# Kernel tuning notes

Measured on AMD Instinct MI355X. Metric: run time of the kernel, lower is better.

Reference implementation:

```python
import jax, jax.numpy as jnp
import numpy as np

B, C, T, N = 8, 128, 64, 256
D_STATE, D_CONV, EXPAND = 4, 3, 1
D_INNER = EXPAND * C
DT_RANK = (C + 15) // 16  # 8


def setup_inputs() -> dict:
    key = jax.random.key(0)
    ks = jax.random.split(key, 8)
    s = lambda k, shape, sc=0.02: jax.random.normal(k, shape, jnp.float32) * sc
    return {
        "x": jax.random.normal(ks[0], (B, C, T, N), jnp.float32),
        "ln_gamma": jnp.ones((C,), jnp.float32),
        "ln_beta": jnp.zeros((C,), jnp.float32),
        "in_proj_w": s(ks[1], (2 * D_INNER, C)),
        "conv_w": s(ks[2], (D_CONV, 1, D_INNER), 0.1),
        "conv_b": jnp.zeros((D_INNER,), jnp.float32),
        "x_proj_w": s(ks[3], (DT_RANK + 2 * D_STATE, D_INNER)),
        "dt_proj_w": s(ks[4], (D_INNER, DT_RANK), 0.1),
        "dt_proj_b": s(ks[5], (D_INNER,), 0.1),
        "A_log": jnp.log(jnp.broadcast_to(jnp.arange(1, D_STATE + 1, dtype=jnp.float32), (D_INNER, D_STATE))),
        "D": jnp.ones((D_INNER,), jnp.float32),
        "out_proj_w": s(ks[6], (C, D_INNER)),
    }


def _mamba(x, in_proj_w, conv_w, conv_b, x_proj_w, dt_proj_w, dt_proj_b, A_log, D, out_proj_w):
    # x: (BN, T, C) -- selective-scan Mamba block, single (forward) direction
    xz = x @ in_proj_w.T                                   # (BN, T, 2*D_INNER)
    xc, z = jnp.split(xz, 2, axis=-1)
    # causal depthwise conv along time
    xp = jnp.pad(xc, ((0, 0), (D_CONV - 1, 0), (0, 0)))
    xc = jax.lax.conv_general_dilated(
        xp, conv_w, (1,), 'VALID',
        dimension_numbers=('NWC', 'WIO', 'NWC'),
        feature_group_count=D_INNER) + conv_b
    xc = jax.nn.silu(xc)
    x_dbl = xc @ x_proj_w.T                                # (BN, T, DT_RANK + 2*D_STATE)
    dt, Bs, Cs = jnp.split(x_dbl, [DT_RANK, DT_RANK + D_STATE], axis=-1)
    dt = jax.nn.softplus(dt @ dt_proj_w.T + dt_proj_b)     # (BN, T, D_INNER)
    A = -jnp.exp(A_log)                                    # (D_INNER, D_STATE)
    dA = jnp.exp(dt[..., None] * A)                        # (BN, T, D_INNER, D_STATE)
    dBx = dt[..., None] * Bs[:, :, None, :] * xc[..., None]

    def step(h, inps):
        dA_t, dBx_t, C_t = inps
        h = h * dA_t + dBx_t                               # (BN, D_INNER, D_STATE)
        y = jnp.einsum('bdn,bn->bd', h, C_t)
        return h, y

    h0 = jnp.zeros((xc.shape[0], D_INNER, D_STATE), xc.dtype)
    _, ys = jax.lax.scan(step, h0, (dA.transpose(1, 0, 2, 3),
                                    dBx.transpose(1, 0, 2, 3),
                                    Cs.transpose(1, 0, 2)))
    y = ys.transpose(1, 0, 2) + xc * D                     # (BN, T, D_INNER)
    y = y * jax.nn.silu(z)                                 # gate (if_divide_out=False)
    return y @ out_proj_w.T


def reference(x, ln_gamma, ln_beta, in_proj_w, conv_w, conv_b, x_proj_w,
              dt_proj_w, dt_proj_b, A_log, D, out_proj_w):
    # (B, C, T, N) -> (B, T, N, C)
    h = x.transpose(0, 2, 3, 1)
    mu = h.mean(-1, keepdims=True)
    var = h.var(-1, keepdims=True)
    h = (h - mu) / jnp.sqrt(var + 1e-5) * ln_gamma + ln_beta
    h = h.astype(jnp.float32)  # fp32 cast (autocast disabled around mamba)
    bb, tt, nn, cc = h.shape
    # temporal mode: each (batch, node) pair is an independent time sequence
    hs = h.transpose(0, 2, 1, 3).reshape(bb * nn, tt, cc)
    y = _mamba(hs, in_proj_w, conv_w, conv_b, x_proj_w, dt_proj_w, dt_proj_b,
               A_log, D, out_proj_w)
    y = y.reshape(bb, nn, tt, cc).transpose(0, 2, 1, 3)    # (B, T, N, C)
    return y.transpose(0, 3, 1, 2)                         # (B, C, T, N)
```

## Files before the change

kernel.cpp:

```cpp
#include <hip/hip_runtime.h>
#include <math.h>

#define B_   8
#define C_   128
#define T_   64
#define N_   256
#define NSEQ 4

typedef __attribute__((ext_vector_type(8))) short bf16x8;
typedef __attribute__((ext_vector_type(4))) float f32x4;
typedef unsigned short ushort_t;

#define LOG2E 1.4426950408889634f
#define LN2   0.6931471805599453f

#define R0   0
#define R1   8448
#define RXD  17024
#define LDSW 18304

#define SELH 0x05040100u
#define SELL 0x07060302u

__device__ __forceinline__ unsigned bfhi(float x) {
  unsigned u = __float_as_uint(x);
  return (u + 0x7FFF + ((u >> 16) & 1)) >> 16;
}
__device__ __forceinline__ unsigned packsplit(float x) {
  unsigned hi = bfhi(x);
  float rem = x - __uint_as_float(hi << 16);
  unsigned lo = bfhi(rem);
  return (hi & 0xFFFFu) | (lo << 16);
}
__device__ __forceinline__ float unpacksplit(unsigned u) {
  return __uint_as_float(u << 16) + __uint_as_float(u & 0xFFFF0000u);
}
__device__ __forceinline__ float fsilu(float v) {
  return v * __builtin_amdgcn_rcpf(1.0f + __builtin_amdgcn_exp2f(-LOG2E * v));
}
__device__ __forceinline__ float qsum4(float v) {
  int x = __builtin_amdgcn_update_dpp(0, __float_as_int(v), 0xB1, 0xF, 0xF, true);
  v += __int_as_float(x);
  x = __builtin_amdgcn_update_dpp(0, __float_as_int(v), 0x4E, 0xF, 0xF, true);
  v += __int_as_float(x);
  return v;
}
__device__ __forceinline__ int sigq(int qk) { return (qk >> 1) | ((qk & 1) << 2); }
__device__ __forceinline__ int kpos(int k, int s) {
  return (k & ~31) + ((((sigq((k >> 2) & 7)) + s) & 7) << 2) + (k & 3);
}
union BU { uint4 q; bf16x8 v; unsigned u[4]; };

__global__ __launch_bounds__(512) void k_wsplit(const float* __restrict__ Win,
                                                const float* __restrict__ Wout,
                                                const float* __restrict__ Wx,
                                                ushort_t* __restrict__ wsi,
                                                ushort_t* __restrict__ wso,
                                                ushort_t* __restrict__ wsx) {
  int idx = blockIdx.x * 512 + threadIdx.x;
  const float* src;
  ushort_t* dst;
  if (idx < 1024) {
    int row = idx >> 2, kc = idx & 3;
    src = Win + row * 128 + kc * 32;
    dst = wsi + (row * 4 + kc) * 64;
  } else if (idx < 1536) {
    int k = idx - 1024;
    int row = k >> 2, kc = k & 3;
    src = Wout + row * 128 + kc * 32;
    dst = wso + (row * 4 + kc) * 64;
  } else if (idx < 1600) {
    int k = idx - 1536;
    int row = k >> 2, kc = k & 3;
    src = Wx + row * 128 + kc * 32;
    dst = wsx + (row * 4 + kc) * 64;
  } else {
    return;
  }
  for (int g = 0; g < 4; ++g) {
    unsigned hw[4], lw[4];
#pragma unroll
    for (int e2 = 0; e2 < 4; ++e2) {
      float x0 = src[g * 8 + 2 * e2], x1 = src[g * 8 + 2 * e2 + 1];
      unsigned p0 = packsplit(x0), p1 = packsplit(x1);
      hw[e2] = (p0 & 0xFFFFu) | (p1 << 16);
      lw[e2] = (p0 >> 16) | (p1 & 0xFFFF0000u);
    }
    *(uint4*)(dst + (g * 2 + 0) * 8) = make_uint4(hw[0], hw[1], hw[2], hw[3]);
    *(uint4*)(dst + (g * 2 + 1) * 8) = make_uint4(lw[0], lw[1], lw[2], lw[3]);
  }
}

__global__ __launch_bounds__(256) void k_ln(const float* __restrict__ x,
                                            const float* __restrict__ gam,
                                            const float* __restrict__ bet,
                                            float* __restrict__ hout) {
  __shared__ float tile[128 * 36];
  __shared__ float ps[8 * 32], pq[8 * 32], mean_s[32], rstd_s[32];
  int bx = blockIdx.x;
  int nt = bx & 7, t = (bx >> 3) & 63, b = bx >> 9;
  int n0 = nt * 32;
  int tid = threadIdx.x;
  const float4* x4 = (const float4*)x;
  for (int it = 0; it < 4; ++it) {
    int idx4 = it * 256 + tid;
    int c = idx4 >> 3, nn4 = idx4 & 7;
    float4 v = x4[((b * C_ + c) * T_ + t) * (N_ / 4) + (n0 >> 2) + nn4];
    *(float4*)&tile[c * 36 + nn4 * 4] = v;
  }
  __syncthreads();
  {
    int nn = tid & 31, cg = tid >> 5;
    float s = 0.f, q = 0.f;
    for (int i = 0; i < 16; ++i) {
      float v = tile[(cg * 16 + i) * 36 + nn];
      s += v; q += v * v;
    }
    ps[cg * 32 + nn] = s; pq[cg * 32 + nn] = q;
  }
  __syncthreads();
  if (tid < 32) {
    float ss = 0.f, qq = 0.f;
    for (int g2 = 0; g2 < 8; ++g2) { ss += ps[g2 * 32 + tid]; qq += pq[g2 * 32 + tid]; }
    float mu = ss * (1.f / 128.f);
    float var = qq * (1.f / 128.f) - mu * mu;
    mean_s[tid] = mu;
    rstd_s[tid] = rsqrtf(var + 1e-5f);
  }
  __syncthreads();
  {
    int c = tid & 127, half = tid >> 7;
    float gm = gam[c], bb = bet[c];
    for (int it = 0; it < 16; ++it) {
      int n = it * 2 + half;
      float v = (tile[c * 36 + n] - mean_s[n]) * rstd_s[n] * gm + bb;
      hout[((b * N_ + n0 + n) * (long)T_ + t) * C_ + c] = v;
    }
  }
}

__global__ __launch_bounds__(512, 4) void k_mamba(
    float* ws,
    const ushort_t* __restrict__ wsi,
    const ushort_t* __restrict__ wso,
    const ushort_t* __restrict__ wsx,
    const float* __restrict__ convw,
    const float* __restrict__ convb,
    const float* __restrict__ Wdt,
    const float* __restrict__ bdt,
    const float* __restrict__ Alog,
    const float* __restrict__ Dp)
{
  extern __shared__ float L[];
  unsigned* Li = (unsigned*)L;
  int tid = threadIdx.x;
  int lane = tid & 63;
  int w = tid >> 6;
  int r16 = lane & 15, g = lane >> 4;
  const uint4* wsi4 = (const uint4*)wsi;
  const uint4* wso4 = (const uint4*)wso;
  const uint4* wsx4 = (const uint4*)wsx;

  uint4 wih[2][4], wil[2][4], woh[4], wol[4];
#pragma unroll
  for (int ci = 0; ci < 2; ++ci)
#pragma unroll
    for (int kc = 0; kc < 4; ++kc) {
      int cb = ((w * 32 + ci * 16 + r16) * 4 + kc) * 8 + g * 2;
      wih[ci][kc] = wsi4[cb];
      wil[ci][kc] = wsi4[cb + 1];
    }
#pragma unroll
  for (int kc = 0; kc < 4; ++kc) {
    int cb = ((w * 16 + r16) * 4 + kc) * 8 + g * 2;
    woh[kc] = wso4[cb];
    wol[kc] = wso4[cb + 1];
  }
  int dc = tid & 127;
  float cw0 = convw[dc], cw1 = convw[128 + dc], cw2 = convw[256 + dc];
  float cbv = convb[dc];
  int ds = tid >> 2, ss = tid & 3;
  float wA = Wdt[ds * 8 + 2 * ss], wB = Wdt[ds * 8 + 2 * ss + 1];
  float bd = bdt[ds];
  float As2 = -expf(Alog[ds * 4 + ss]) * LOG2E;
  float Dd = Dp[ds];
  int kc_d = (ds & ~31) + (ds & 3);
  int qs_d = sigq((ds >> 2) & 7);

  for (int iseq = 0; iseq < NSEQ; ++iseq) {
    float* hseq = ws + ((long)blockIdx.x * NSEQ + iseq) * (T_ * C_);

    {
      const float4* h4 = (const float4*)hseq;
      int ts = tid >> 3, kg = tid & 7;
      int s = ts & 7;
      int slot = (sigq(kg) + s) & 7;
#pragma unroll
      for (int q = 0; q < 4; ++q) {
        float4 v = h4[ts * 32 + kg + 8 * q];
        uint4 pw = make_uint4(packsplit(v.x), packsplit(v.y), packsplit(v.z), packsplit(v.w));
        *(uint4*)&Li[R0 + ts * 132 + q * 32 + slot * 4] = pw;
      }
    }
    __syncthreads();

    f32x4 acc[4][2];
#pragma unroll
    for (int rt = 0; rt < 4; ++rt)
#pragma unroll
      for (int ci = 0; ci < 2; ++ci) acc[rt][ci] = (f32x4){0.f, 0.f, 0.f, 0.f};
    {
      int s = r16 & 7;
      int slotA = (g + s) & 7, slotB = (g + 4 + s) & 7;
#pragma unroll
      for (int kc = 0; kc < 4; ++kc) {
#pragma unroll
        for (int rt = 0; rt < 4; ++rt) {
          int base = R0 + (rt * 16 + r16) * 132 + kc * 32;
          uint4 wa = *(const uint4*)&Li[base + slotA * 4];
          uint4 wb = *(const uint4*)&Li[base + slotB * 4];
          BU ah, al;
          ah.u[0] = __builtin_amdgcn_perm(wa.y, wa.x, SELH);
          ah.u[1] = __builtin_amdgcn_perm(wa.w, wa.z, SELH);
          ah.u[2] = __builtin_amdgcn_perm(wb.y, wb.x, SELH);
          ah.u[3] = __builtin_amdgcn_perm(wb.w, wb.z, SELH);
          al.u[0] = __builtin_amdgcn_perm(wa.y, wa.x, SELL);
          al.u[1] = __builtin_amdgcn_perm(wa.w, wa.z, SELL);
          al.u[2] = __builtin_amdgcn_perm(wb.y, wb.x, SELL);
          al.u[3] = __builtin_amdgcn_perm(wb.w, wb.z, SELL);
#pragma unroll
          for (int ci = 0; ci < 2; ++ci) {
            BU bh, bl;
            bh.q = wih[ci][kc];
            bl.q = wil[ci][kc];
            acc[rt][ci] = __builtin_amdgcn_mfma_f32_16x16x32_bf16(al.v, bh.v, acc[rt][ci], 0, 0, 0);
            acc[rt][ci] = __builtin_amdgcn_mfma_f32_16x16x32_bf16(ah.v, bl.v, acc[rt][ci], 0, 0, 0);
            acc[rt][ci] = __builtin_amdgcn_mfma_f32_16x16x32_bf16(ah.v, bh.v, acc[rt][ci], 0, 0, 0);
          }
        }
      }
    }
    __syncthreads();

    {
      int dl0 = (w & 3) * 32;
      if (w < 4) {
#pragma unroll
        for (int rt = 0; rt < 4; ++rt)
#pragma unroll
          for (int ci = 0; ci < 2; ++ci)
#pragma unroll
            for (int r = 0; r < 4; ++r)
              L[R0 + (rt * 16 + g * 4 + r) * 132 + dl0 + ci * 16 + r16] = acc[rt][ci][r];
      } else {
#pragma unroll
        for (int rt = 0; rt < 4; ++rt)
#pragma unroll
          for (int ci = 0; ci < 2; ++ci)
#pragma unroll
            for (int r = 0; r < 4; ++r)
              L[R1 + (dl0 + ci * 16 + r16) * 67 + rt * 16 + g * 4 + r] = fsilu(acc[rt][ci][r]);
      }
    }
    __syncthreads();

    {
      int tq = tid >> 7;
      int t0 = tq * 16;
      float xin[18];
#pragma unroll
      for (int ii = 0; ii < 18; ++ii) {
        int t = t0 - 2 + ii;
        xin[ii] = (t < 0) ? 0.f : L[R0 + t * 132 + dc];
      }
      __syncthreads();
#pragma unroll
      for (int ii = 0; ii < 16; ++ii) {
        int t = t0 + ii;
        float v = fmaf(cw2, xin[ii + 2], fmaf(cw1, xin[ii + 1], fmaf(cw0, xin[ii], cbv)));
        Li[R0 + t * 132 + kpos(dc, t & 7)] = packsplit(fsilu(v));
      }
    }
    __syncthreads();

    if (w < 4) {
      int s = r16 & 7;
      int slotA = (g + s) & 7, slotB = (g + 4 + s) & 7;
      f32x4 o = (f32x4){0.f, 0.f, 0.f, 0.f};
#pragma unroll
      for (int kc = 0; kc < 4; ++kc) {
        int cb = (r16 * 4 + kc) * 8 + g * 2;
        BU bh, bl;
        bh.q = wsx4[cb];
        bl.q = wsx4[cb + 1];
        int base = R0 + (w * 16 + r16) * 132 + kc * 32;
        uint4 wa = *(const uint4*)&Li[base + slotA * 4];
        uint4 wb = *(const uint4*)&Li[base + slotB * 4];
        BU ah, al;
        ah.u[0] = __builtin_amdgcn_perm(wa.y, wa.x, SELH);
        ah.u[1] = __builtin_amdgcn_perm(wa.w, wa.z, SELH);
        ah.u[2] = __builtin_amdgcn_perm(wb.y, wb.x, SELH);
        ah.u[3] = __builtin_amdgcn_perm(wb.w, wb.z, SELH);
        al.u[0] = __builtin_amdgcn_perm(wa.y, wa.x, SELL);
        al.u[1] = __builtin_amdgcn_perm(wa.w, wa.z, SELL);
        al.u[2] = __builtin_amdgcn_perm(wb.y, wb.x, SELL);
        al.u[3] = __builtin_amdgcn_perm(wb.w, wb.z, SELL);
        o = __builtin_amdgcn_mfma_f32_16x16x32_bf16(al.v, bh.v, o, 0, 0, 0);
        o = __builtin_amdgcn_mfma_f32_16x16x32_bf16(ah.v, bl.v, o, 0, 0, 0);
        o = __builtin_amdgcn_mfma_f32_16x16x32_bf16(ah.v, bh.v, o, 0, 0, 0);
      }
      int p = (r16 < 8) ? ((r16 >> 1) * 4 + (r16 & 1))
                        : (r16 < 12 ? (r16 - 8) * 4 + 2 : (r16 - 12) * 4 + 3);
#pragma unroll
      for (int q = 0; q < 4; ++q)
        L[RXD + (w * 16 + g * 4 + q) * 20 + p] = o[q];
    }
    __syncthreads();

    {
      float h = 0.f;
#pragma unroll 8
      for (int t = 0; t < 64; ++t) {
        float4 xd = *(const float4*)&L[RXD + t * 20 + ss * 4];
        float dtv = qsum4(fmaf(xd.x, wA, xd.y * wB)) + bd;
        float e = __builtin_amdgcn_exp2f(dtv * LOG2E);
        float sp = LN2 * __builtin_amdgcn_logf(1.0f + e);
        dtv = (dtv > 20.f) ? dtv : sp;
        int xoff = R0 + t * 132 + kc_d + (((qs_d + (t & 7)) & 7) << 2);
        float xcv = unpacksplit(Li[xoff]);
        float dA = __builtin_amdgcn_exp2f(dtv * As2);
        h = fmaf(h, dA, dtv * xcv * xd.z);
        float y = qsum4(h * xd.w);
        if ((t & 3) == ss) {
          y = fmaf(xcv, Dd, y);
          y *= L[R1 + ds * 67 + t];
          Li[xoff] = packsplit(y);
        }
      }
    }
    __syncthreads();

    {
      int s = r16 & 7;
      int slotA = (g + s) & 7, slotB = (g + 4 + s) & 7;
      f32x4 o[4];
#pragma unroll
      for (int rt = 0; rt < 4; ++rt) o[rt] = (f32x4){0.f, 0.f, 0.f, 0.f};
#pragma unroll
      for (int kc = 0; kc < 4; ++kc) {
        BU bh, bl;
        bh.q = woh[kc];
        bl.q = wol[kc];
#pragma unroll
        for (int rt = 0; rt < 4; ++rt) {
          int base = R0 + (rt * 16 + r16) * 132 + kc * 32;
          uint4 wa = *(const uint4*)&Li[base + slotA * 4];
          uint4 wb = *(const uint4*)&Li[base + slotB * 4];
          BU ah, al;
          ah.u[0] = __builtin_amdgcn_perm(wa.y, wa.x, SELH);
          ah.u[1] = __builtin_amdgcn_perm(wa.w, wa.z, SELH);
          ah.u[2] = __builtin_amdgcn_perm(wb.y, wb.x, SELH);
          ah.u[3] = __builtin_amdgcn_perm(wb.w, wb.z, SELH);
          al.u[0] = __builtin_amdgcn_perm(wa.y, wa.x, SELL);
          al.u[1] = __builtin_amdgcn_perm(wa.w, wa.z, SELL);
          al.u[2] = __builtin_amdgcn_perm(wb.y, wb.x, SELL);
          al.u[3] = __builtin_amdgcn_perm(wb.w, wb.z, SELL);
          o[rt] = __builtin_amdgcn_mfma_f32_16x16x32_bf16(al.v, bh.v, o[rt], 0, 0, 0);
          o[rt] = __builtin_amdgcn_mfma_f32_16x16x32_bf16(ah.v, bl.v, o[rt], 0, 0, 0);
          o[rt] = __builtin_amdgcn_mfma_f32_16x16x32_bf16(ah.v, bh.v, o[rt], 0, 0, 0);
        }
      }
#pragma unroll
      for (int rt = 0; rt < 4; ++rt)
#pragma unroll
        for (int r = 0; r < 4; ++r)
          hseq[(rt * 16 + g * 4 + r) * C_ + w * 16 + r16] = o[rt][r];
    }
    __syncthreads();
  }
}

__global__ __launch_bounds__(256) void k_out_tr(const float* __restrict__ ws_y,
                                                float* __restrict__ out) {
  __shared__ float tile[32 * 132];
  int bx = blockIdx.x;
  int nt = bx & 7, t = (bx >> 3) & 63, b = bx >> 9;
  int n0 = nt * 32;
  int tid = threadIdx.x;
  const float4* y4 = (const float4*)ws_y;
  for (int it = 0; it < 4; ++it) {
    int idx4 = it * 256 + tid;
    int nn = idx4 >> 5, c4 = idx4 & 31;
    float4 v = y4[((b * N_ + n0 + nn) * (long)T_ + t) * (C_ / 4) + c4];
    *(float4*)&tile[nn * 132 + c4 * 4] = v;
  }
  __syncthreads();
  int nn = tid & 31, cg = tid >> 5;
  for (int i = 0; i < 16; ++i) {
    int c = cg * 16 + i;
    out[((b * C_ + c) * (long)T_ + t) * N_ + n0 + nn] = tile[nn * 132 + c];
  }
}

extern "C" void kernel_launch(void* const* d_in, const int* in_sizes, int n_in,
                              void* d_out, int out_size, void* d_ws, size_t ws_size,
                              hipStream_t stream) {
  const float* x    = (const float*)d_in[0];
  const float* gam  = (const float*)d_in[1];
  const float* bet  = (const float*)d_in[2];
  const float* Win  = (const float*)d_in[3];
  const float* cw   = (const float*)d_in[4];
  const float* cb   = (const float*)d_in[5];
  const float* Wx   = (const float*)d_in[6];
  const float* Wdt  = (const float*)d_in[7];
  const float* bdt  = (const float*)d_in[8];
  const float* Alog = (const float*)d_in[9];
  const float* Dp   = (const float*)d_in[10];
  const float* Wout = (const float*)d_in[11];
  float* out = (float*)d_out;
  float* ws  = (float*)d_ws;

  const size_t HBYTES = 67108864ull;
  const size_t WBYTES = 131072ull + 65536ull + 8192ull;
  char* wtail;
  if (ws_size >= HBYTES + WBYTES) wtail = (char*)d_ws + HBYTES;
  else                            wtail = (char*)d_out;
  ushort_t* wsi = (ushort_t*)wtail;
  ushort_t* wso = (ushort_t*)(wtail + 131072);
  ushort_t* wsx = (ushort_t*)(wtail + 131072 + 65536);

  (void)hipFuncSetAttribute((const void*)k_mamba,
                            hipFuncAttributeMaxDynamicSharedMemorySize,
                            LDSW * 4);

  k_wsplit<<<4, 512, 0, stream>>>(Win, Wout, Wx, wsi, wso, wsx);
  k_ln<<<4096, 256, 0, stream>>>(x, gam, bet, ws);
  k_mamba<<<2048 / NSEQ, 512, LDSW * 4, stream>>>(ws, wsi, wso, wsx, cw, cb,
                                                  Wdt, bdt, Alog, Dp);
  k_out_tr<<<4096, 256, 0, stream>>>(ws, out);
}
```

Before: 238.0 us.

## Split hi/lo bf16 planes in LDS, restructure dt computation and scan, reload weights

The input tile is now stored as separate hi and lo bf16 planes in LDS with a padded row stride, so the in-projection MFMA operands load directly without perm-based unpacking. The dt projection is computed once per timestep by one lane of each quad, using all 8 weights, and then broadcast through DPP, replacing the per-step qsum4 reduction. The low halves of the in-proj weights and all out-proj weights are reloaded from global memory inside the loop instead of being held in registers, which lowers register pressure but adds global loads. The x_dbl layout in LDS is simplified to match.

```diff
diff --git a/kernel.cpp b/kernel.cpp
--- a/kernel.cpp
+++ b/kernel.cpp
@@ -14,10 +14,11 @@
 #define LOG2E 1.4426950408889634f
 #define LN2   0.6931471805599453f
 
-#define R0   0
-#define R1   8448
-#define RXD  17024
-#define LDSW 18304
+#define RH   0
+#define RL   4352
+#define R1   8704
+#define RXD  17280
+#define LDSW 18560
 
 #define SELH 0x05040100u
 #define SELL 0x07060302u
@@ -44,6 +45,11 @@
   x = __builtin_amdgcn_update_dpp(0, __float_as_int(v), 0x4E, 0xF, 0xF, true);
   v += __int_as_float(x);
   return v;
+}
+template <int SI>
+__device__ __forceinline__ float qbcast(float v) {
+  constexpr int sel = SI | (SI << 2) | (SI << 4) | (SI << 6);
+  return __int_as_float(__builtin_amdgcn_update_dpp(0, __float_as_int(v), sel, 0xF, 0xF, true));
 }
 __device__ __forceinline__ int sigq(int qk) { return (qk >> 1) | ((qk & 1) << 2); }
 __device__ __forceinline__ int kpos(int k, int s) {
@@ -161,26 +167,19 @@
   const uint4* wso4 = (const uint4*)wso;
   const uint4* wsx4 = (const uint4*)wsx;
 
-  uint4 wih[2][4], wil[2][4], woh[4], wol[4];
+  uint4 wih[2][4];
 #pragma unroll
   for (int ci = 0; ci < 2; ++ci)
 #pragma unroll
-    for (int kc = 0; kc < 4; ++kc) {
-      int cb = ((w * 32 + ci * 16 + r16) * 4 + kc) * 8 + g * 2;
-      wih[ci][kc] = wsi4[cb];
-      wil[ci][kc] = wsi4[cb + 1];
-    }
-#pragma unroll
-  for (int kc = 0; kc < 4; ++kc) {
-    int cb = ((w * 16 + r16) * 4 + kc) * 8 + g * 2;
-    woh[kc] = wso4[cb];
-    wol[kc] = wso4[cb + 1];
-  }
+    for (int kc = 0; kc < 4; ++kc)
+      wih[ci][kc] = wsi4[((w * 32 + ci * 16 + r16) * 4 + kc) * 8 + g * 2];
+
   int dc = tid & 127;
   float cw0 = convw[dc], cw1 = convw[128 + dc], cw2 = convw[256 + dc];
   float cbv = convb[dc];
   int ds = tid >> 2, ss = tid & 3;
-  float wA = Wdt[ds * 8 + 2 * ss], wB = Wdt[ds * 8 + 2 * ss + 1];
+  float4 wdta = *(const float4*)&Wdt[ds * 8];
+  float4 wdtb = *(const float4*)&Wdt[ds * 8 + 4];
   float bd = bdt[ds];
   float As2 = -expf(Alog[ds * 4 + ss]) * LOG2E;
   float Dd = Dp[ds];
@@ -193,14 +192,24 @@
     {
       const float4* h4 = (const float4*)hseq;
       int ts = tid >> 3, kg = tid & 7;
-      int s = ts & 7;
-      int slot = (sigq(kg) + s) & 7;
+      unsigned hw[8], lw[8];
 #pragma unroll
       for (int q = 0; q < 4; ++q) {
-        float4 v = h4[ts * 32 + kg + 8 * q];
-        uint4 pw = make_uint4(packsplit(v.x), packsplit(v.y), packsplit(v.z), packsplit(v.w));
-        *(uint4*)&Li[R0 + ts * 132 + q * 32 + slot * 4] = pw;
-      }
+        float4 v = h4[ts * 32 + kg * 4 + q];
+        unsigned h0 = bfhi(v.x), h1 = bfhi(v.y), h2 = bfhi(v.z), h3 = bfhi(v.w);
+        hw[2 * q]     = h0 | (h1 << 16);
+        hw[2 * q + 1] = h2 | (h3 << 16);
+        float r0 = v.x - __uint_as_float(h0 << 16);
+        float r1 = v.y - __uint_as_float(h1 << 16);
+        float r2 = v.z - __uint_as_float(h2 << 16);
+        float r3 = v.w - __uint_as_float(h3 << 16);
+        lw[2 * q]     = bfhi(r0) | (bfhi(r1) << 16);
+        lw[2 * q + 1] = bfhi(r2) | (bfhi(r3) << 16);
+      }
+      *(uint4*)&Li[RH + ts * 68 + kg * 8]     = make_uint4(hw[0], hw[1], hw[2], hw[3]);
+      *(uint4*)&Li[RH + ts * 68 + kg * 8 + 4] = make_uint4(hw[4], hw[5], hw[6], hw[7]);
+      *(uint4*)&Li[RL + ts * 68 + kg * 8]     = make_uint4(lw[0], lw[1], lw[2], lw[3]);
+      *(uint4*)&Li[RL + ts * 68 + kg * 8 + 4] = make_uint4(lw[4], lw[5], lw[6], lw[7]);
     }
     __syncthreads();
 
@@ -209,35 +218,25 @@
     for (int rt = 0; rt < 4; ++rt)
 #pragma unroll
       for (int ci = 0; ci < 2; ++ci) acc[rt][ci] = (f32x4){0.f, 0.f, 0.f, 0.f};
-    {
-      int s = r16 & 7;
-      int slotA = (g + s) & 7, slotB = (g + 4 + s) & 7;
-#pragma unroll
-      for (int kc = 0; kc < 4; ++kc) {
-#pragma unroll
-        for (int rt = 0; rt < 4; ++rt) {
-          int base = R0 + (rt * 16 + r16) * 132 + kc * 32;
-          uint4 wa = *(const uint4*)&Li[base + slotA * 4];
-          uint4 wb = *(const uint4*)&Li[base + slotB * 4];
-          BU ah, al;
-          ah.u[0] = __builtin_amdgcn_perm(wa.y, wa.x, SELH);
-          ah.u[1] = __builtin_amdgcn_perm(wa.w, wa.z, SELH);
-          ah.u[2] = __builtin_amdgcn_perm(wb.y, wb.x, SELH);
-          ah.u[3] = __builtin_amdgcn_perm(wb.w, wb.z, SELH);
-          al.u[0] = __builtin_amdgcn_perm(wa.y, wa.x, SELL);
-          al.u[1] = __builtin_amdgcn_perm(wa.w, wa.z, SELL);
-          al.u[2] = __builtin_amdgcn_perm(wb.y, wb.x, SELL);
-          al.u[3] = __builtin_amdgcn_perm(wb.w, wb.z, SELL);
-#pragma unroll
-          for (int ci = 0; ci < 2; ++ci) {
-            BU bh, bl;
-            bh.q = wih[ci][kc];
-            bl.q = wil[ci][kc];
-            acc[rt][ci] = __builtin_amdgcn_mfma_f32_16x16x32_bf16(al.v, bh.v, acc[rt][ci], 0, 0, 0);
-            acc[rt][ci] = __builtin_amdgcn_mfma_f32_16x16x32_bf16(ah.v, bl.v, acc[rt][ci], 0, 0, 0);
-            acc[rt][ci] = __builtin_amdgcn_mfma_f32_16x16x32_bf16(ah.v, bh.v, acc[rt][ci], 0, 0, 0);
-          }
-        }
+#pragma unroll
+    for (int kc = 0; kc < 4; ++kc) {
+      BU bl0, bl1, bh0, bh1;
+      bl0.q = wsi4[((w * 32 + r16) * 4 + kc) * 8 + g * 2 + 1];
+      bl1.q = wsi4[((w * 32 + 16 + r16) * 4 + kc) * 8 + g * 2 + 1];
+      bh0.q = wih[0][kc];
+      bh1.q = wih[1][kc];
+#pragma unroll
+      for (int rt = 0; rt < 4; ++rt) {
+        int row = rt * 16 + r16;
+        BU ah, al;
+        ah.q = *(const uint4*)&Li[RH + row * 68 + kc * 16 + g * 4];
+        al.q = *(const uint4*)&Li[RL + row * 68 + kc * 16 + g * 4];
+        acc[rt][0] = __builtin_amdgcn_mfma_f32_16x16x32_bf16(al.v, bh0.v, acc[rt][0], 0, 0, 0);
+        acc[rt][0] = __builtin_amdgcn_mfma_f32_16x16x32_bf16(ah.v, bl0.v, acc[rt][0], 0, 0, 0);
+        acc[rt][0] = __builtin_amdgcn_mfma_f32_16x16x32_bf16(ah.v, bh0.v, acc[rt][0], 0, 0, 0);
+        acc[rt][1] = __builtin_amdgcn_mfma_f32_16x16x32_bf16(al.v, bh1.v, acc[rt][1], 0, 0, 0);
+        acc[rt][1] = __builtin_amdgcn_mfma_f32_16x16x32_bf16(ah.v, bl1.v, acc[rt][1], 0, 0, 0);
+        acc[rt][1] = __builtin_amdgcn_mfma_f32_16x16x32_bf16(ah.v, bh1.v, acc[rt][1], 0, 0, 0);
       }
     }
     __syncthreads();
@@ -251,7 +250,7 @@
           for (int ci = 0; ci < 2; ++ci)
 #pragma unroll
             for (int r = 0; r < 4; ++r)
-              L[R0 + (rt * 16 + g * 4 + r) * 132 + dl0 + ci * 16 + r16] = acc[rt][ci][r];
+              L[(rt * 16 + g * 4 + r) * 132 + dl0 + ci * 16 + r16] = acc[rt][ci][r];
       } else {
 #pragma unroll
         for (int rt = 0; rt < 4; ++rt)
@@ -271,14 +270,14 @@
 #pragma unroll
       for (int ii = 0; ii < 18; ++ii) {
         int t = t0 - 2 + ii;
-        xin[ii] = (t < 0) ? 0.f : L[R0 + t * 132 + dc];
+        xin[ii] = (t < 0) ? 0.f : L[t * 132 + dc];
       }
       __syncthreads();
 #pragma unroll
       for (int ii = 0; ii < 16; ++ii) {
         int t = t0 + ii;
         float v = fmaf(cw2, xin[ii + 2], fmaf(cw1, xin[ii + 1], fmaf(cw0, xin[ii], cbv)));
-        Li[R0 + t * 132 + kpos(dc, t & 7)] = packsplit(fsilu(v));
+        Li[t * 132 + kpos(dc, t & 7)] = packsplit(fsilu(v));
       }
     }
     __syncthreads();
@@ -293,7 +292,7 @@
         BU bh, bl;
         bh.q = wsx4[cb];
         bl.q = wsx4[cb + 1];
-        int base = R0 + (w * 16 + r16) * 132 + kc * 32;
+        int base = (w * 16 + r16) * 132 + kc * 32;
         uint4 wa = *(const uint4*)&Li[base + slotA * 4];
         uint4 wb = *(const uint4*)&Li[base + slotB * 4];
         BU ah, al;
@@ -309,33 +308,51 @@
         o = __builtin_amdgcn_mfma_f32_16x16x32_bf16(ah.v, bl.v, o, 0, 0, 0);
         o = __builtin_amdgcn_mfma_f32_16x16x32_bf16(ah.v, bh.v, o, 0, 0, 0);
       }
-      int p = (r16 < 8) ? ((r16 >> 1) * 4 + (r16 & 1))
-                        : (r16 < 12 ? (r16 - 8) * 4 + 2 : (r16 - 12) * 4 + 3);
 #pragma unroll
       for (int q = 0; q < 4; ++q)
-        L[RXD + (w * 16 + g * 4 + q) * 20 + p] = o[q];
+        L[RXD + (w * 16 + g * 4 + q) * 20 + r16] = o[q];
     }
     __syncthreads();
 
     {
-      float h = 0.f;
-#pragma unroll 8
-      for (int t = 0; t < 64; ++t) {
-        float4 xd = *(const float4*)&L[RXD + t * 20 + ss * 4];
-        float dtv = qsum4(fmaf(xd.x, wA, xd.y * wB)) + bd;
-        float e = __builtin_amdgcn_exp2f(dtv * LOG2E);
+      float hsv = 0.f;
+#pragma unroll
+      for (int tb = 0; tb < 16; ++tb) {
+        int tme = tb * 4 + ss;
+        const float* xr = &L[RXD + tme * 20];
+        float4 xa = *(const float4*)xr;
+        float4 xb = *(const float4*)(xr + 4);
+        float dot = bd;
+        dot = fmaf(xa.x, wdta.x, dot); dot = fmaf(xa.y, wdta.y, dot);
+        dot = fmaf(xa.z, wdta.z, dot); dot = fmaf(xa.w, wdta.w, dot);
+        dot = fmaf(xb.x, wdtb.x, dot); dot = fmaf(xb.y, wdtb.y, dot);
+        dot = fmaf(xb.z, wdtb.z, dot); dot = fmaf(xb.w, wdtb.w, dot);
+        float e = __builtin_amdgcn_exp2f(dot * LOG2E);
         float sp = LN2 * __builtin_amdgcn_logf(1.0f + e);
-        dtv = (dtv > 20.f) ? dtv : sp;
-        int xoff = R0 + t * 132 + kc_d + (((qs_d + (t & 7)) & 7) << 2);
-        float xcv = unpacksplit(Li[xoff]);
-        float dA = __builtin_amdgcn_exp2f(dtv * As2);
-        h = fmaf(h, dA, dtv * xcv * xd.z);
-        float y = qsum4(h * xd.w);
-        if ((t & 3) == ss) {
-          y = fmaf(xcv, Dd, y);
-          y *= L[R1 + ds * 67 + t];
-          Li[xoff] = packsplit(y);
+        float dtme = (dot > 20.f) ? dot : sp;
+
+#define SCANSTEP(SI)                                                          \
+        {                                                                     \
+          int t = tb * 4 + SI;                                                \
+          float dtv = qbcast<SI>(dtme);                                       \
+          float Bs = L[RXD + t * 20 + 8 + ss];                                \
+          float Cs = L[RXD + t * 20 + 12 + ss];                               \
+          int xoff = t * 132 + kc_d + (((qs_d + (t & 7)) & 7) << 2);          \
+          float xcv = unpacksplit(Li[xoff]);                                  \
+          float dA = __builtin_amdgcn_exp2f(dtv * As2);                       \
+          hsv = fmaf(hsv, dA, dtv * xcv * Bs);                                \
+          float y = qsum4(hsv * Cs);                                          \
+          if (SI == ss) {                                                     \
+            y = fmaf(xcv, Dd, y);                                             \
+            y *= L[R1 + ds * 67 + t];                                         \
+            Li[xoff] = packsplit(y);                                          \
+          }                                                                   \
         }
+        SCANSTEP(0)
+        SCANSTEP(1)
+        SCANSTEP(2)
+        SCANSTEP(3)
+#undef SCANSTEP
       }
     }
     __syncthreads();
@@ -348,12 +365,13 @@
       for (int rt = 0; rt < 4; ++rt) o[rt] = (f32x4){0.f, 0.f, 0.f, 0.f};
 #pragma unroll
       for (int kc = 0; kc < 4; ++kc) {
+        int cb = ((w * 16 + r16) * 4 + kc) * 8 + g * 2;
         BU bh, bl;
-        bh.q = woh[kc];
-        bl.q = wol[kc];
+        bh.q = wso4[cb];
+        bl.q = wso4[cb + 1];
 #pragma unroll
         for (int rt = 0; rt < 4; ++rt) {
-          int base = R0 + (rt * 16 + r16) * 132 + kc * 32;
+          int base = (rt * 16 + r16) * 132 + kc * 32;
           uint4 wa = *(const uint4*)&Li[base + slotA * 4];
           uint4 wb = *(const uint4*)&Li[base + slotB * 4];
           BU ah, al;
```

Measured after the change: 556.0 us. 2.34x slower.
